# Kernel tuning notes

Measured on AMD Instinct MI355X. Metric: run time of the kernel, lower is better.

The kernel has to match this reference:

```python
import jax, jax.numpy as jnp
import numpy as np

C, K, DIL = 128, 3, 1
PAD = DIL
KK = K * K
EPS = 1e-5


def setup_inputs() -> dict:
    key = jax.random.key(0)
    k0, k1, k2 = jax.random.split(key, 3)
    B, H, W = 8, 128, 128
    x = jax.random.normal(k0, (B, C, H, W), jnp.float32)
    # small offset-conv weights so predicted offsets are realistic (sub-pixel scale)
    w_off = jax.random.normal(k1, (2 * KK, C, K, K), jnp.float32) * 0.01
    b_off = jnp.zeros((2 * KK,), jnp.float32)
    w_dw = jax.random.normal(k2, (C, 1, K, K), jnp.float32) * (1.0 / 3.0)
    gamma = jnp.ones((C,), jnp.float32)
    beta = jnp.zeros((C,), jnp.float32)
    return {"x": x, "w_off": w_off, "b_off": b_off, "w_dw": w_dw,
            "gamma": gamma, "beta": beta}


def _deform_depthwise(x, offset, w_dw):
    """torchvision-style deform_conv2d, groups=C (depthwise), stride=1."""
    B, C_, H, W = x.shape
    off = offset.reshape(B, KK, 2, H, W)  # (y,x) pairs per kernel tap
    hs = jnp.arange(H, dtype=x.dtype)[None, None, :, None]
    ws = jnp.arange(W, dtype=x.dtype)[None, None, None, :]
    ki = jnp.arange(K, dtype=x.dtype)
    ky = jnp.repeat(ki, K)  # [KK] row index of tap
    kx = jnp.tile(ki, K)    # [KK] col index of tap
    # sampling positions: base grid + dilated tap offset - pad + learned offset
    py = hs + (DIL * ky - PAD)[None, :, None, None] + off[:, :, 0]  # [B,KK,H,W]
    px = ws + (DIL * kx - PAD)[None, :, None, None] + off[:, :, 1]
    y0 = jnp.floor(py)
    x0 = jnp.floor(px)
    ty = py - y0
    tx = px - x0
    y0i = y0.astype(jnp.int32)
    x0i = x0.astype(jnp.int32)

    def gather(xb, yi, xi):
        # zero outside the image (torchvision zero-pad semantics)
        valid = (yi >= 0) & (yi < H) & (xi >= 0) & (xi < W)
        yc = jnp.clip(yi, 0, H - 1)
        xc = jnp.clip(xi, 0, W - 1)
        v = xb[:, yc, xc]  # [C,KK,H,W]
        return v * valid[None].astype(xb.dtype)

    def sample_one(xb, y0b, x0b, tyb, txb):
        v00 = gather(xb, y0b, x0b)
        v01 = gather(xb, y0b, x0b + 1)
        v10 = gather(xb, y0b + 1, x0b)
        v11 = gather(xb, y0b + 1, x0b + 1)
        w00 = (1 - tyb) * (1 - txb)
        w01 = (1 - tyb) * txb
        w10 = tyb * (1 - txb)
        w11 = tyb * txb
        return (v00 * w00[None] + v01 * w01[None]
                + v10 * w10[None] + v11 * w11[None])  # [C,KK,H,W]

    val = jax.vmap(sample_one)(x, y0i, x0i, ty, tx)  # [B,C,KK,H,W]
    # depthwise contraction over the KK taps
    return jnp.einsum('bckhw,ck->bchw', val, w_dw.reshape(C, KK))


def reference(x, w_off, b_off, w_dw, gamma, beta):
    identity = x
    offset = jax.lax.conv_general_dilated(
        x, w_off, window_strides=(1, 1), padding=[(PAD, PAD), (PAD, PAD)],
        dimension_numbers=('NCHW', 'OIHW', 'NCHW'))
    offset = offset + b_off[None, :, None, None]
    out = _deform_depthwise(x, offset, w_dw)
    # BatchNorm2d in training mode (batch statistics), then SiLU
    mean = jnp.mean(out, axis=(0, 2, 3), keepdims=True)
    var = jnp.mean((out - mean) ** 2, axis=(0, 2, 3), keepdims=True)
    out = (out - mean) * jax.lax.rsqrt(var + EPS)
    out = out * gamma[None, :, None, None] + beta[None, :, None, None]
    out = out * jax.nn.sigmoid(out)  # SiLU
    return out + identity
```

## Files before the change

kernel.cpp:

```cpp
#include <hip/hip_runtime.h>
#include <hip/hip_fp16.h>
#include <math.h>

#define Cc 128
#define Hh 128
#define Ww 128
#define Bb 8
#define HW 16384
#define NPIX 131072
#define NOFF 18

typedef unsigned int u32;
typedef _Float16 half8 __attribute__((ext_vector_type(8)));
typedef __attribute__((ext_vector_type(16))) float f32x16;

static __device__ __forceinline__ u32 pack2h(float a, float b){
  __half2 h = __floats2half2_rn(a, b);
  return *(u32*)&h;
}

__global__ __launch_bounds__(256) void k_repack(const float* __restrict__ w_off, const float* __restrict__ w_dw,
                                                u32* __restrict__ wBf, u32* __restrict__ wdt_h){
  int i = blockIdx.x*256 + threadIdx.x;
  if (i < 72*64*4){
    int step = i >> 8;
    int r    = i & 255;
    int lane = r >> 2;
    int q    = r & 3;
    int tap  = step / 8, chunk = step % 8;
    int o    = lane & 31, half = lane >> 5;
    int c0   = chunk*16 + half*8 + 2*q;
    float v0 = (o < NOFF) ? w_off[(size_t)(o*Cc + c0    )*9 + tap] : 0.f;
    float v1 = (o < NOFF) ? w_off[(size_t)(o*Cc + c0 + 1)*9 + tap] : 0.f;
    wBf[i] = pack2h(v0, v1);
  }
  int j = i - 72*64*4;
  if (j >= 0 && j < 9*64){
    int cp = j & 63; int k = j >> 6;
    wdt_h[j] = pack2h(w_dw[(2*cp)*9 + k], w_dw[(2*cp+1)*9 + k]);
  }
}

__global__ __launch_bounds__(256) void k_tx(const float* __restrict__ x, u32* __restrict__ xt16){
  __shared__ float t[128][65];
  int tid = threadIdx.x;
  int b   = blockIdx.x >> 8;
  int hw0 = (blockIdx.x & 255) << 6;
  int lane = tid & 63, wg = tid >> 6;
  const float* xb = x + (size_t)b*Cc*HW;
  #pragma unroll
  for (int k=0;k<32;k++){
    int c = wg + k*4;
    t[c][lane] = xb[(size_t)c*HW + hw0 + lane];
  }
  __syncthreads();
  u32* ob = xt16 + ((size_t)b*HW + hw0)*64;
  int cpair = tid & 63, grp = tid >> 6;
  #pragma unroll
  for (int k=0;k<16;k++){
    int hwl = grp + k*4;
    ob[(size_t)hwl*64 + cpair] = pack2h(t[cpair*2][hwl], t[cpair*2+1][hwl]);
  }
}

__global__ __launch_bounds__(128) void k_offset_mfma(const u32* __restrict__ xt, const u32* __restrict__ wBf,
                                                     const float* __restrict__ b_off, u32* __restrict__ recs){
  __shared__ u32 xl[3][68][65];
  float* pivf = (float*)&xl[0][0][0];
  int tid = threadIdx.x, lane = tid & 63, wv = tid >> 6;
  int b  = blockIdx.x >> 8;
  int rm = blockIdx.x & 255;
  int h  = rm >> 1, wh = rm & 1;
  int row = lane & 31, half = lane >> 5;
  int w = wh*64 + wv*32 + row;
  int w0c = wh*64 - 2;

  const u32* xb = xt + (size_t)b*HW*64;

  for (int i = tid; i < 3*68*16; i += 128){
    int q = i & 15; int t2 = i >> 4; int p = t2 % 68; int r = t2 / 68;
    int hh = min(max(h + r - 1, 0), Hh-1);
    int gc = min(max(w0c + p, 0), Ww-1);
    *(uint4*)&xl[r][p][q*4] = *(const uint4*)(xb + ((size_t)(hh*Ww + gc))*64 + q*4);
  }
  __syncthreads();

  bool tval[9]; int tpd[9];
  #pragma unroll
  for (int t=0;t<9;t++){
    int ky = t/3 - 1, dx = t%3 - 1;
    int hh = h + ky, wt = w + dx;
    tval[t] = (hh>=0)&&(hh<Hh)&&(wt>=0)&&(wt<Ww);
    int p = wv*32 + row + 2 + dx;
    tpd[t] = (t/3)*4420 + p*65 + half*4;
  }

  f32x16 accE, accO;
  #pragma unroll
  for (int i=0;i<16;i++){ accE[i]=0.f; accO[i]=0.f; }

  const u32* xl0 = &xl[0][0][0];
  const uint4* wb = (const uint4*)wBf;
  #pragma unroll 1
  for (int t=0;t<9;t++){
    bool v = tval[t];
    int base = tpd[t];
    #pragma unroll
    for (int ch=0;ch<8;ch++){
      uint4 a = *(const uint4*)(xl0 + base + ch*8);
      if (!v){ a.x=0u; a.y=0u; a.z=0u; a.w=0u; }
      uint4 bf = wb[(t*8+ch)*64 + lane];
      if (ch & 1) accO = __builtin_amdgcn_mfma_f32_32x32x16_f16(*(half8*)&a, *(half8*)&bf, accO, 0, 0, 0);
      else        accE = __builtin_amdgcn_mfma_f32_32x32x16_f16(*(half8*)&a, *(half8*)&bf, accE, 0, 0, 0);
    }
  }
  f32x16 acc = accE + accO;

  __syncthreads();

  int o = lane & 31;
  #pragma unroll
  for (int r=0;r<16;r++){
    int pxl = wv*32 + ((r&3) + 8*(r>>2) + 4*half);
    if (o < NOFF) pivf[pxl*21 + o] = acc[r];
  }
  __syncthreads();

  if (tid < 64){
    int wpx = wh*64 + tid;
    float v[NOFF];
    #pragma unroll
    for (int oo=0;oo<NOFF;oo++) v[oo] = pivf[tid*21 + oo] + b_off[oo];

    u32 rec[36];
    #pragma unroll
    for (int kk=0;kk<9;kk++){
      float py = (float)(h + kk/3 - 1) + v[2*kk];
      float qx = (float)(wpx + kk%3 - 1) + v[2*kk+1];
      float fy = floorf(py), fx = floorf(qx);
      float ty = py - fy, tx = qx - fx;
      int y0 = (int)fy, x0 = (int)fx;
      int y1 = y0+1, x1 = x0+1;
      bool vy0 = (y0>=0)&&(y0<Hh), vy1=(y1>=0)&&(y1<Hh);
      bool vx0 = (x0>=0)&&(x0<Ww), vx1=(x1>=0)&&(x1<Ww);
      u32 yc0 = (u32)(min(max(y0,0),Hh-1)*Ww), yc1 = (u32)(min(max(y1,0),Hh-1)*Ww);
      u32 xc0 = (u32)min(max(x0,0),Ww-1),      xc1 = (u32)min(max(x1,0),Ww-1);
      rec[2*kk]   = (yc0+xc0) | ((yc0+xc1)<<16);
      rec[2*kk+1] = (yc1+xc0) | ((yc1+xc1)<<16);
      float c00 = (vy0&&vx0) ? (1.f-ty)*(1.f-tx) : 0.f;
      float c01 = (vy0&&vx1) ? (1.f-ty)*tx       : 0.f;
      float c10 = (vy1&&vx0) ? ty*(1.f-tx)       : 0.f;
      float c11 = (vy1&&vx1) ? ty*tx             : 0.f;
      rec[18+2*kk] = pack2h(c00, c01);
      rec[19+2*kk] = pack2h(c10, c11);
    }
    int pxg = b*HW + h*Ww + wpx;
    uint4* dst = (uint4*)(recs + (size_t)pxg*36);
    #pragma unroll
    for (int q=0;q<9;q++) dst[q] = *(uint4*)(rec + q*4);
  }
}

template<bool F16OUT>
__global__ __launch_bounds__(256) void k_deform_rec(const u32* __restrict__ xt, const u32* __restrict__ recs,
                                                    const u32* __restrict__ wdt_h, float* __restrict__ out,
                                                    u32* __restrict__ dwb, float* __restrict__ bps){
  __shared__ float pivot[16][132];
  int tid = threadIdx.x, lane = tid & 63, wid = tid >> 6;
  int pxb = blockIdx.x * 16;
  int bu = pxb >> 14, hw0 = pxb & 16383;
  int l2 = lane*2;

  __half2 wk2[9];
  #pragma unroll
  for (int k=0;k<9;k++){
    u32 wv = wdt_h[k*64 + lane];
    wk2[k] = *(__half2*)&wv;
  }

  const u32* xbu = xt + (size_t)bu*HW*64;

  #pragma unroll
  for (int i=0;i<4;i++){
    int pu = __builtin_amdgcn_readfirstlane(pxb + wid*4 + i);
    const u32* rec = recs + (size_t)pu*36;

    u32 q[9][4];
    #pragma unroll
    for (int kk=0;kk<9;kk++){
      u32 dA = rec[2*kk], dB = rec[2*kk+1];
      q[kk][0] = xbu[(size_t)(dA & 0xFFFFu)*64 + lane];
      q[kk][1] = xbu[(size_t)(dA >> 16)   *64 + lane];
      q[kk][2] = xbu[(size_t)(dB & 0xFFFFu)*64 + lane];
      q[kk][3] = xbu[(size_t)(dB >> 16)   *64 + lane];
    }

    __half2 acc2 = __floats2half2_rn(0.f, 0.f);
    #pragma unroll
    for (int kk=0;kk<9;kk++){
      u32 uA = rec[18+2*kk], uB = rec[19+2*kk];
      __half2 hA = *(__half2*)&uA, hB = *(__half2*)&uB;
      __half2 q0 = *(__half2*)&q[kk][0], q1 = *(__half2*)&q[kk][1];
      __half2 q2 = *(__half2*)&q[kk][2], q3 = *(__half2*)&q[kk][3];
      __half2 s = __hmul2(__low2half2(hA), q0);
      s = __hfma2(__high2half2(hA), q1, s);
      s = __hfma2(__low2half2(hB),  q2, s);
      s = __hfma2(__high2half2(hB), q3, s);
      acc2 = __hfma2(wk2[kk], s, acc2);
    }
    pivot[wid*4+i][l2]   = __low2float(acc2);
    pivot[wid*4+i][l2+1] = __high2float(acc2);
  }
  __syncthreads();
  #pragma unroll
  for (int it=0; it<2; it++){
    int c = (tid>>2) + it*64, qd = tid & 3;
    float4 r = make_float4(pivot[qd*4+0][c], pivot[qd*4+1][c], pivot[qd*4+2][c], pivot[qd*4+3][c]);
    float s  = (r.x + r.y) + (r.z + r.w);
    float s2 = fmaf(r.x,r.x, fmaf(r.y,r.y, fmaf(r.z,r.z, r.w*r.w)));
    s  += __shfl_down(s, 2, 4);  s  += __shfl_down(s, 1, 4);
    s2 += __shfl_down(s2, 2, 4); s2 += __shfl_down(s2, 1, 4);
    if (qd == 0){
      bps[(size_t)blockIdx.x*256 + c]       = s;
      bps[(size_t)blockIdx.x*256 + 128 + c] = s2;
    }
    if (F16OUT){
      uint2 pp; pp.x = pack2h(r.x, r.y); pp.y = pack2h(r.z, r.w);
      *(uint2*)&dwb[(((size_t)bu*Cc + c)*HW + hw0)/2 + qd*2] = pp;
    } else {
      *(float4*)(out + ((size_t)bu*Cc + c)*HW + hw0 + qd*4) = r;
    }
  }
}

__global__ __launch_bounds__(256) void k_statsr1(const float* __restrict__ bps, float* __restrict__ part2){
  int tid = threadIdx.x;
  size_t base = (size_t)blockIdx.x * 64;
  float a = 0.f;
  for (int r=0;r<64;r++) a += bps[(base + r)*256 + tid];
  part2[blockIdx.x*256 + tid] = a;
}

__global__ __launch_bounds__(256) void k_statsr2(const float* __restrict__ part2, float* __restrict__ mr){
  __shared__ float t[256];
  int tid = threadIdx.x;
  float a = 0.f;
  for (int r=0;r<128;r++) a += part2[r*256 + tid];
  t[tid] = a;
  __syncthreads();
  if (tid < 128){
    float S = t[tid], S2 = t[128 + tid];
    const float invN = 1.f/(float)(Bb*HW);
    float m = S*invN;
    float var = S2*invN - m*m;
    mr[tid]       = m;
    mr[Cc + tid]  = rsqrtf(var + 1e-5f);
  }
}

__global__ __launch_bounds__(256) void k_apply_f32(float* __restrict__ out, const float* __restrict__ x,
                                                   const float* __restrict__ mr, const float* __restrict__ gamma,
                                                   const float* __restrict__ beta){
  int i = blockIdx.x*256 + threadIdx.x;
  int c = (i >> 12) & 127;
  float4 v  = ((const float4*)out)[i];
  float4 xi = ((const float4*)x)[i];
  float m = mr[c], r = mr[Cc+c], g = gamma[c], be = beta[c];
  float* vp = (float*)&v; const float* xp = (const float*)&xi;
  float4 o; float* op = (float*)&o;
  #pragma unroll
  for (int j=0;j<4;j++){
    float t = (vp[j]-m)*r*g + be;
    t = t / (1.f + expf(-t));
    op[j] = t + xp[j];
  }
  ((float4*)out)[i] = o;
}

__global__ __launch_bounds__(256) void k_apply_f16(const u32* __restrict__ dwb, float* __restrict__ out,
                                                   const float* __restrict__ x, const float* __restrict__ mr,
                                                   const float* __restrict__ gamma, const float* __restrict__ beta){
  int i = blockIdx.x*256 + threadIdx.x;
  int c = (i >> 12) & 127;
  uint2 dw = ((const uint2*)dwb)[i];
  float4 xi = ((const float4*)x)[i];
  float m = mr[c], r = mr[Cc+c], g = gamma[c], be = beta[c];
  __half2 d0 = *(__half2*)&dw.x, d1 = *(__half2*)&dw.y;
  float v[4];
  v[0] = __low2float(d0); v[1] = __high2float(d0);
  v[2] = __low2float(d1); v[3] = __high2float(d1);
  const float* xp = (const float*)&xi;
  float4 o; float* op = (float*)&o;
  #pragma unroll
  for (int j=0;j<4;j++){
    float t = (v[j]-m)*r*g + be;
    t = t / (1.f + expf(-t));
    op[j] = t + xp[j];
  }
  ((float4*)out)[i] = o;
}

extern "C" void kernel_launch(void* const* d_in, const int* in_sizes, int n_in,
                              void* d_out, int out_size, void* d_ws, size_t ws_size,
                              hipStream_t stream) {
  const float* x     = (const float*)d_in[0];
  const float* w_off = (const float*)d_in[1];
  const float* b_off = (const float*)d_in[2];
  const float* w_dw  = (const float*)d_in[3];
  const float* gamma = (const float*)d_in[4];
  const float* beta  = (const float*)d_in[5];
  float* out = (float*)d_out;

  u32*   wBf  = (u32*)d_ws;
  u32*   wdt_h= (u32*)d_ws + 23040;
  float* mr   = (float*)d_ws + 24576;
  u32*   recs = (u32*)d_ws + 32768;
  u32*   xt16 = recs + (size_t)NPIX*36;
  float* bps  = (float*)(xt16 + (size_t)NPIX*64);
  float* part2= bps + (size_t)8192*256;
  u32*   dwb  = (u32*)(part2 + 128*256);

  const size_t NEED_B = ((size_t)32768 + (size_t)NPIX*36 + (size_t)NPIX*64
                         + (size_t)8192*256 + 128*256 + (size_t)NPIX*64) * 4;
  bool big = (ws_size >= NEED_B);

  hipLaunchKernelGGL(k_repack, dim3((72*64*4 + 9*64 + 255)/256), dim3(256), 0, stream, w_off, w_dw, wBf, wdt_h);
  hipLaunchKernelGGL(k_tx,     dim3(2048), dim3(256), 0, stream, x, xt16);
  hipLaunchKernelGGL(k_offset_mfma, dim3(2048), dim3(128), 0, stream, xt16, wBf, b_off, recs);

  if (big){
    hipLaunchKernelGGL((k_deform_rec<true>), dim3(NPIX/16), dim3(256), 0, stream, xt16, recs, wdt_h, out, dwb, bps);
  } else {
    hipLaunchKernelGGL((k_deform_rec<false>), dim3(NPIX/16), dim3(256), 0, stream, xt16, recs, wdt_h, out, dwb, bps);
  }
  hipLaunchKernelGGL(k_statsr1, dim3(128), dim3(256), 0, stream, bps, part2);
  hipLaunchKernelGGL(k_statsr2, dim3(1),   dim3(256), 0, stream, part2, mr);
  if (big){
    hipLaunchKernelGGL(k_apply_f16, dim3(NPIX*Cc/4/256), dim3(256), 0, stream, dwb, out, x, mr, gamma, beta);
  } else {
    hipLaunchKernelGGL(k_apply_f32, dim3(NPIX*Cc/4/256), dim3(256), 0, stream, out, x, mr, gamma, beta);
  }
}
```

Measured before the change: 173.3 us.

## Process full image row per block and stream input rows through shared memory

```diff
diff --git a/kernel.cpp b/kernel.cpp
--- a/kernel.cpp
+++ b/kernel.cpp
@@ -63,61 +63,55 @@
   }
 }
 
-__global__ __launch_bounds__(128) void k_offset_mfma(const u32* __restrict__ xt, const u32* __restrict__ wBf,
+__global__ __launch_bounds__(256) void k_offset_mfma(const u32* __restrict__ xt, const u32* __restrict__ wBf,
                                                      const float* __restrict__ b_off, u32* __restrict__ recs){
-  __shared__ u32 xl[3][68][65];
-  float* pivf = (float*)&xl[0][0][0];
+  __shared__ u32 xl[132][65];
   int tid = threadIdx.x, lane = tid & 63, wv = tid >> 6;
-  int b  = blockIdx.x >> 8;
-  int rm = blockIdx.x & 255;
-  int h  = rm >> 1, wh = rm & 1;
+  int b = blockIdx.x >> 7, h = blockIdx.x & 127;
   int row = lane & 31, half = lane >> 5;
-  int w = wh*64 + wv*32 + row;
-  int w0c = wh*64 - 2;
+  int w = wv*32 + row;
 
   const u32* xb = xt + (size_t)b*HW*64;
-
-  for (int i = tid; i < 3*68*16; i += 128){
-    int q = i & 15; int t2 = i >> 4; int p = t2 % 68; int r = t2 / 68;
-    int hh = min(max(h + r - 1, 0), Hh-1);
-    int gc = min(max(w0c + p, 0), Ww-1);
-    *(uint4*)&xl[r][p][q*4] = *(const uint4*)(xb + ((size_t)(hh*Ww + gc))*64 + q*4);
-  }
-  __syncthreads();
-
-  bool tval[9]; int tpd[9];
-  #pragma unroll
-  for (int t=0;t<9;t++){
-    int ky = t/3 - 1, dx = t%3 - 1;
-    int hh = h + ky, wt = w + dx;
-    tval[t] = (hh>=0)&&(hh<Hh)&&(wt>=0)&&(wt<Ww);
-    int p = wv*32 + row + 2 + dx;
-    tpd[t] = (t/3)*4420 + p*65 + half*4;
-  }
+  const uint4* wb = (const uint4*)wBf;
 
   f32x16 accE, accO;
   #pragma unroll
   for (int i=0;i<16;i++){ accE[i]=0.f; accO[i]=0.f; }
 
-  const u32* xl0 = &xl[0][0][0];
-  const uint4* wb = (const uint4*)wBf;
+  const u32* xl0 = &xl[0][0];
+
   #pragma unroll 1
-  for (int t=0;t<9;t++){
-    bool v = tval[t];
-    int base = tpd[t];
-    #pragma unroll
-    for (int ch=0;ch<8;ch++){
-      uint4 a = *(const uint4*)(xl0 + base + ch*8);
-      if (!v){ a.x=0u; a.y=0u; a.z=0u; a.w=0u; }
-      uint4 bf = wb[(t*8+ch)*64 + lane];
-      if (ch & 1) accO = __builtin_amdgcn_mfma_f32_32x32x16_f16(*(half8*)&a, *(half8*)&bf, accO, 0, 0, 0);
-      else        accE = __builtin_amdgcn_mfma_f32_32x32x16_f16(*(half8*)&a, *(half8*)&bf, accE, 0, 0, 0);
+  for (int r=0; r<3; r++){
+    int hh = h + r - 1;
+    int hc = min(max(hh,0),Hh-1);
+    __syncthreads();
+    for (int i=tid; i<132*16; i+=256){
+      int q = i & 15, p = i >> 4;
+      int gc = min(max(p-2, 0), Ww-1);
+      *(uint4*)&xl[p][q*4] = *(const uint4*)(xb + ((size_t)(hc*Ww + gc))*64 + q*4);
+    }
+    __syncthreads();
+    bool rowv = (hh>=0)&&(hh<Hh);
+    #pragma unroll
+    for (int dx=0; dx<3; dx++){
+      int t = r*3 + dx;
+      int wt = w + dx - 1;
+      bool v = rowv && (wt>=0)&&(wt<Ww);
+      int base = (w + dx + 1)*65 + half*4;
+      #pragma unroll
+      for (int ch=0; ch<8; ch++){
+        uint4 a = *(const uint4*)(xl0 + base + ch*8);
+        if (!v){ a.x=0u; a.y=0u; a.z=0u; a.w=0u; }
+        uint4 bf = wb[(t*8+ch)*64 + lane];
+        if (ch & 1) accO = __builtin_amdgcn_mfma_f32_32x32x16_f16(*(half8*)&a, *(half8*)&bf, accO, 0, 0, 0);
+        else        accE = __builtin_amdgcn_mfma_f32_32x32x16_f16(*(half8*)&a, *(half8*)&bf, accE, 0, 0, 0);
+      }
     }
   }
   f32x16 acc = accE + accO;
 
   __syncthreads();
-
+  float* pivf = (float*)&xl[0][0];
   int o = lane & 31;
   #pragma unroll
   for (int r=0;r<16;r++){
@@ -126,8 +120,8 @@
   }
   __syncthreads();
 
-  if (tid < 64){
-    int wpx = wh*64 + tid;
+  if (tid < 128){
+    int wpx = tid;
     float v[NOFF];
     #pragma unroll
     for (int oo=0;oo<NOFF;oo++) v[oo] = pivf[tid*21 + oo] + b_off[oo];
@@ -326,7 +320,7 @@
 
   hipLaunchKernelGGL(k_repack, dim3((72*64*4 + 9*64 + 255)/256), dim3(256), 0, stream, w_off, w_dw, wBf, wdt_h);
   hipLaunchKernelGGL(k_tx,     dim3(2048), dim3(256), 0, stream, x, xt16);
-  hipLaunchKernelGGL(k_offset_mfma, dim3(2048), dim3(128), 0, stream, xt16, wBf, b_off, recs);
+  hipLaunchKernelGGL(k_offset_mfma, dim3(1024), dim3(256), 0, stream, xt16, wBf, b_off, recs);
 
   if (big){
     hipLaunchKernelGGL((k_deform_rec<true>), dim3(NPIX/16), dim3(256), 0, stream, xt16, recs, wdt_h, out, dwb, bps);
```

Result: faster. 156.2 us (median of 2 runs) (-9.9%).
